# Kernel tuning notes

Hardware: AMD Instinct MI355X
Metric: run time of the kernel (lower is better)

Reference implementation:

```python
import jax, jax.numpy as jnp
import numpy as np

N = 4096  # seq_len (input feature dim, per nn.Linear(seq_len, d))
D = 4096  # d; note forward only type-checks when n_rows(x) == d
SCALE = 1.0 / np.sqrt(np.float32(D))


def setup_inputs() -> dict:
    key = jax.random.key(0)
    ks = jax.random.split(key, 7)
    w_std = np.float32(1.0 / np.sqrt(N))  # ~ torch Linear init scale
    return {
        "x": jax.random.normal(ks[0], (D, N), dtype=jnp.float32),
        "Wq": jax.random.normal(ks[1], (N, D), dtype=jnp.float32) * w_std,
        "bq": jax.random.normal(ks[2], (D,), dtype=jnp.float32) * w_std,
        "Wk": jax.random.normal(ks[3], (N, D), dtype=jnp.float32) * w_std,
        "bk": jax.random.normal(ks[4], (D,), dtype=jnp.float32) * w_std,
        "Wv": jax.random.normal(ks[5], (N, D), dtype=jnp.float32) * w_std,
        "bv": jax.random.normal(ks[6], (D,), dtype=jnp.float32) * w_std,
    }


def reference(x, Wq, bq, Wk, bk, Wv, bv):
    # q, k, v: [T, D] with T == D (required by the original code's shapes)
    q = x @ Wq + bq
    k = x @ Wk + bk
    v = x @ Wv + bv
    # full T x T score matrix, scaled by sqrt(d)
    scores = (q @ k.T) * SCALE
    # F.softmax with no dim on a 2-D tensor -> dim=1 (rows)
    p = jax.nn.softmax(scores, axis=-1)
    # NOTE: original multiplies by v TRANSPOSED (P @ v.T), kept faithfully
    return p @ v.T
```

## Files before the change

kernel.cpp:

```cpp
#include <hip/hip_runtime.h>

#define MAT_N 4096
#define SM ((size_t)MAT_N * (size_t)MAT_N)

typedef __bf16 bf16_t;
typedef __bf16 bf16x8 __attribute__((ext_vector_type(8)));
typedef float f32x4 __attribute__((ext_vector_type(4)));

__device__ __forceinline__ unsigned short f2bf_bits(float f) {
  unsigned u = __builtin_bit_cast(unsigned, f);
  u += 0x7fffu + ((u >> 16) & 1u);
  return (unsigned short)(u >> 16);
}
__device__ __forceinline__ bf16_t f2bf(float f) {
  unsigned short s = f2bf_bits(f);
  return __builtin_bit_cast(bf16_t, s);
}
__device__ __forceinline__ float bf2f(unsigned short b) {
  unsigned u = ((unsigned)b) << 16;
  return __builtin_bit_cast(float, u);
}

__device__ __forceinline__ void gl_lds16(const bf16_t* g, bf16_t* l) {
  __builtin_amdgcn_global_load_lds(
      (const __attribute__((address_space(1))) void*)g,
      (__attribute__((address_space(3))) void*)l, 16, 0, 0);
}

__global__ __launch_bounds__(256) void prep_kernel(
    const float* __restrict__ x, const float* __restrict__ W0,
    const float* __restrict__ W1, const float* __restrict__ W2,
    bf16_t* __restrict__ xb, bf16_t* __restrict__ WT) {
  const int r = threadIdx.x / 16;
  const int c4 = (threadIdx.x % 16) * 4;
  const int z = blockIdx.z;
  if (z == 3) {
    const int row0 = blockIdx.y * 64, col0 = blockIdx.x * 64;
#pragma unroll
    for (int i = 0; i < 4; ++i) {
      int rr = row0 + r + i * 16;
      float4 v = *(const float4*)(x + (size_t)rr * MAT_N + col0 + c4);
      ushort4 u;
      u.x = f2bf_bits(v.x);
      u.y = f2bf_bits(v.y);
      u.z = f2bf_bits(v.z);
      u.w = f2bf_bits(v.w);
      *(ushort4*)((unsigned short*)xb + (size_t)rr * MAT_N + col0 + c4) = u;
    }
    return;
  }
  const float* W = (z == 0) ? W0 : (z == 1 ? W1 : W2);
  bf16_t* T = WT + (size_t)z * SM;
  __shared__ float tile[64][65];
  const int n0 = blockIdx.y * 64;
  const int d0 = blockIdx.x * 64;
#pragma unroll
  for (int i = 0; i < 4; ++i) {
    int rr = r + i * 16;
    float4 v = *(const float4*)(W + (size_t)(n0 + rr) * MAT_N + d0 + c4);
    tile[rr][c4 + 0] = v.x;
    tile[rr][c4 + 1] = v.y;
    tile[rr][c4 + 2] = v.z;
    tile[rr][c4 + 3] = v.w;
  }
  __syncthreads();
#pragma unroll
  for (int i = 0; i < 4; ++i) {
    int rr = r + i * 16;
    ushort4 u;
    u.x = f2bf_bits(tile[c4 + 0][rr]);
    u.y = f2bf_bits(tile[c4 + 1][rr]);
    u.z = f2bf_bits(tile[c4 + 2][rr]);
    u.w = f2bf_bits(tile[c4 + 3][rr]);
    *(ushort4*)((unsigned short*)T + (size_t)(d0 + rr) * MAT_N + n0 + c4) = u;
  }
}

template <int EPI>
__global__ __launch_bounds__(256, 4) void gemm_nt_kernel(
    const bf16_t* __restrict__ A, const bf16_t* __restrict__ B,
    const float* __restrict__ b0, const float* __restrict__ b1,
    const float* __restrict__ b2, void* __restrict__ Cv,
    float* __restrict__ l, float scale) {
  __shared__ bf16_t As[128 * 32];
  __shared__ bf16_t Bs[128 * 32];
  const int t = threadIdx.x;
  const int wave = t >> 6;
  const int lane = t & 63;
  const int quad = lane >> 4;
  const int lrow = lane & 15;
  const int m0 = blockIdx.y * 128;
  const int n0 = blockIdx.x * 128;
  const int wm = (wave >> 1) * 64;
  const int wn = (wave & 1) * 64;

  const int srow = t >> 2;
  const int scol = (t & 3) * 8;
  const bf16_t* ga = A + (size_t)(m0 + srow) * MAT_N + scol;
  const bf16_t* gb = B + (size_t)(n0 + srow) * MAT_N + scol;
  bf16_t* lA0 = As + wave * 512;
  bf16_t* lB0 = Bs + wave * 512;

  f32x4 acc[4][4];
#pragma unroll
  for (int r = 0; r < 4; ++r)
#pragma unroll
    for (int c = 0; c < 4; ++c) acc[r][c] = (f32x4)0.f;

  for (int k0 = 0; k0 < MAT_N; k0 += 32, ga += 32, gb += 32) {
    gl_lds16(ga, lA0);
    gl_lds16(ga + (size_t)64 * MAT_N, lA0 + 2048);
    gl_lds16(gb, lB0);
    gl_lds16(gb + (size_t)64 * MAT_N, lB0 + 2048);
    __syncthreads();

    bf16x8 af[4];
#pragma unroll
    for (int r = 0; r < 4; ++r)
      af[r] = *(const bf16x8*)(As + (wm + r * 16 + lrow) * 32 + quad * 8);
#pragma unroll
    for (int c = 0; c < 4; ++c) {
      bf16x8 bfc = *(const bf16x8*)(Bs + (wn + c * 16 + lrow) * 32 + quad * 8);
#pragma unroll
      for (int r = 0; r < 4; ++r)
        acc[r][c] = __builtin_amdgcn_mfma_f32_16x16x32_bf16(af[r], bfc,
                                                            acc[r][c], 0, 0, 0);
    }
    __syncthreads();
  }

  if (EPI == 0) {
    const int z = n0 >> 12;
    const int nn0 = n0 & 4095;
    const float* bias = (z == 0) ? b0 : (z == 1 ? b1 : b2);
    bf16_t* C = (bf16_t*)Cv + (size_t)z * SM;
#pragma unroll
    for (int c = 0; c < 4; ++c) {
      const int col = nn0 + wn + c * 16 + lrow;
      const float bv = bias[col];
#pragma unroll
      for (int r = 0; r < 4; ++r) {
        const int rowb = m0 + wm + r * 16 + quad * 4;
#pragma unroll
        for (int reg = 0; reg < 4; ++reg)
          C[(size_t)(rowb + reg) * MAT_N + col] = f2bf(acc[r][c][reg] + bv);
      }
    }
  } else if (EPI == 1) {
    unsigned short* C = (unsigned short*)Cv;
#pragma unroll
    for (int r = 0; r < 4; ++r) {
#pragma unroll
      for (int reg = 0; reg < 4; ++reg) {
        const int row = m0 + wm + r * 16 + quad * 4 + reg;
        float s = 0.f;
#pragma unroll
        for (int c = 0; c < 4; ++c) {
          const int col = n0 + wn + c * 16 + lrow;
          float e = __expf(acc[r][c][reg] * scale);
          unsigned short eb = f2bf_bits(e);
          C[(size_t)row * MAT_N + col] = eb;
          s += bf2f(eb);
        }
        s += __shfl_xor(s, 1);
        s += __shfl_xor(s, 2);
        s += __shfl_xor(s, 4);
        s += __shfl_xor(s, 8);
        if (lrow == 0) atomicAdd(&l[row], s);
      }
    }
  } else {
    float* C = (float*)Cv;
#pragma unroll
    for (int r = 0; r < 4; ++r) {
#pragma unroll
      for (int reg = 0; reg < 4; ++reg) {
        const int row = m0 + wm + r * 16 + quad * 4 + reg;
        const float inv = 1.0f / l[row];
#pragma unroll
        for (int c = 0; c < 4; ++c) {
          const int col = n0 + wn + c * 16 + lrow;
          C[(size_t)row * MAT_N + col] = acc[r][c][reg] * inv;
        }
      }
    }
  }
}

extern "C" void kernel_launch(void* const* d_in, const int* in_sizes, int n_in,
                              void* d_out, int out_size, void* d_ws,
                              size_t ws_size, hipStream_t stream) {
  const float* x = (const float*)d_in[0];
  const float* Wq = (const float*)d_in[1];
  const float* bq = (const float*)d_in[2];
  const float* Wk = (const float*)d_in[3];
  const float* bk = (const float*)d_in[4];
  const float* Wv = (const float*)d_in[5];
  const float* bv = (const float*)d_in[6];
  float* out = (float*)d_out;

  const size_t SB = 2 * SM;
  char* ws = (char*)d_ws;
  bf16_t* xb = (bf16_t*)(ws);
  bf16_t* pb = (bf16_t*)(ws);
  bf16_t* WT = (bf16_t*)(ws + SB);
  float* lrow = (float*)(ws + SB);
  bf16_t* qkv = (bf16_t*)(ws + 4 * SB);

  const dim3 blk(256);
  prep_kernel<<<dim3(64, 64, 4), blk, 0, stream>>>(x, Wq, Wk, Wv, xb, WT);
  gemm_nt_kernel<0><<<dim3(96, 32), blk, 0, stream>>>(
      xb, WT, bq, bk, bv, qkv, nullptr, 0.f);
  hipMemsetAsync(lrow, 0, MAT_N * sizeof(float), stream);
  gemm_nt_kernel<1><<<dim3(32, 32), blk, 0, stream>>>(
      qkv, qkv + SM, nullptr, nullptr, nullptr, pb, lrow, 0.015625f);
  gemm_nt_kernel<2><<<dim3(32, 32), blk, 0, stream>>>(
      pb, qkv + 2 * SM, nullptr, nullptr, nullptr, out, lrow, 1.f);
}
```

Baseline: 1.080 ms.

## Double the K-step per barrier and add grouped block-index swizzle

The GEMM main loop now loads two 32-wide K slices per iteration into enlarged shared buffers. This halves the number of __syncthreads barriers and gives more MFMA work per load phase. Block indices are also remapped into groups of 8 row-tiles so that concurrently running blocks share A/B tiles in L2. Shared memory per block doubles to 32KB, which may limit occupancy against the launch bound of 4 blocks.

```diff
diff --git a/kernel.cpp b/kernel.cpp
--- a/kernel.cpp
+++ b/kernel.cpp
@@ -82,15 +82,25 @@
     const float* __restrict__ b0, const float* __restrict__ b1,
     const float* __restrict__ b2, void* __restrict__ Cv,
     float* __restrict__ l, float scale) {
-  __shared__ bf16_t As[128 * 32];
-  __shared__ bf16_t Bs[128 * 32];
+  __shared__ bf16_t As[2 * 128 * 32];
+  __shared__ bf16_t Bs[2 * 128 * 32];
   const int t = threadIdx.x;
   const int wave = t >> 6;
   const int lane = t & 63;
   const int quad = lane >> 4;
   const int lrow = lane & 15;
-  const int m0 = blockIdx.y * 128;
-  const int n0 = blockIdx.x * 128;
+
+  const int nbx = gridDim.x, nby = gridDim.y;
+  const int pid = blockIdx.y * nbx + blockIdx.x;
+  const int G = 8;
+  const int span = G * nbx;
+  const int group = pid / span;
+  const int first = group * G;
+  const int gsz = min(G, nby - first);
+  const int rem = pid - group * span;
+  const int m0 = (first + rem % gsz) * 128;
+  const int n0 = (rem / gsz) * 128;
+
   const int wm = (wave >> 1) * 64;
   const int wn = (wave & 1) * 64;
 
@@ -98,8 +108,10 @@
   const int scol = (t & 3) * 8;
   const bf16_t* ga = A + (size_t)(m0 + srow) * MAT_N + scol;
   const bf16_t* gb = B + (size_t)(n0 + srow) * MAT_N + scol;
-  bf16_t* lA0 = As + wave * 512;
-  bf16_t* lB0 = Bs + wave * 512;
+  const bf16_t* ga2 = ga + (size_t)64 * MAT_N;
+  const bf16_t* gb2 = gb + (size_t)64 * MAT_N;
+  bf16_t* lA = As + wave * 512;
+  bf16_t* lB = Bs + wave * 512;
 
   f32x4 acc[4][4];
 #pragma unroll
@@ -107,24 +119,35 @@
 #pragma unroll
     for (int c = 0; c < 4; ++c) acc[r][c] = (f32x4)0.f;
 
-  for (int k0 = 0; k0 < MAT_N; k0 += 32, ga += 32, gb += 32) {
-    gl_lds16(ga, lA0);
-    gl_lds16(ga + (size_t)64 * MAT_N, lA0 + 2048);
-    gl_lds16(gb, lB0);
-    gl_lds16(gb + (size_t)64 * MAT_N, lB0 + 2048);
+  for (int k0 = 0; k0 < MAT_N; k0 += 64) {
+    gl_lds16(ga, lA);
+    gl_lds16(ga2, lA + 2048);
+    gl_lds16(ga + 32, lA + 4096);
+    gl_lds16(ga2 + 32, lA + 6144);
+    gl_lds16(gb, lB);
+    gl_lds16(gb2, lB + 2048);
+    gl_lds16(gb + 32, lB + 4096);
+    gl_lds16(gb2 + 32, lB + 6144);
+    ga += 64; ga2 += 64; gb += 64; gb2 += 64;
     __syncthreads();
 
-    bf16x8 af[4];
-#pragma unroll
-    for (int r = 0; r < 4; ++r)
-      af[r] = *(const bf16x8*)(As + (wm + r * 16 + lrow) * 32 + quad * 8);
-#pragma unroll
-    for (int c = 0; c < 4; ++c) {
-      bf16x8 bfc = *(const bf16x8*)(Bs + (wn + c * 16 + lrow) * 32 + quad * 8);
+#pragma unroll
+    for (int s = 0; s < 2; ++s) {
+      const bf16_t* Ab = As + s * 4096;
+      const bf16_t* Bb = Bs + s * 4096;
+      bf16x8 af[4];
 #pragma unroll
       for (int r = 0; r < 4; ++r)
-        acc[r][c] = __builtin_amdgcn_mfma_f32_16x16x32_bf16(af[r], bfc,
-                                                            acc[r][c], 0, 0, 0);
+        af[r] = *(const bf16x8*)(Ab + (wm + r * 16 + lrow) * 32 + quad * 8);
+#pragma unroll
+      for (int c = 0; c < 4; ++c) {
+        bf16x8 bfc =
+            *(const bf16x8*)(Bb + (wn + c * 16 + lrow) * 32 + quad * 8);
+#pragma unroll
+        for (int r = 0; r < 4; ++r)
+          acc[r][c] = __builtin_amdgcn_mfma_f32_16x16x32_bf16(
+              af[r], bfc, acc[r][c], 0, 0, 0);
+      }
     }
     __syncthreads();
   }
```

Result: faster. 1.055 ms (-2.3%).
